# Optimization experiments

Hardware: AMD Instinct MI355X
Metric: run time of the kernel (lower is better)

The kernel has to match this reference:

```python
import jax, jax.numpy as jnp
import numpy as np

B, S, D, H = 4, 2048, 1024, 16
PD = D // H  # projection (head) dim


def setup_inputs() -> dict:
    key = jax.random.key(0)
    ks = jax.random.split(key, 11)
    s = 1.0 / np.sqrt(D)
    return {
        "q": jax.random.normal(ks[0], (B, S, D), jnp.float32),
        "k": jax.random.normal(ks[1], (B, S, D), jnp.float32),
        "v": jax.random.normal(ks[2], (B, S, D), jnp.float32),
        "Wq": jax.random.normal(ks[3], (D, D), jnp.float32) * s,
        "bq": jnp.zeros((D,), jnp.float32),
        "Wk": jax.random.normal(ks[4], (D, D), jnp.float32) * s,
        "bk": jnp.zeros((D,), jnp.float32),
        "Wv": jax.random.normal(ks[5], (D, D), jnp.float32) * s,
        "bv": jnp.zeros((D,), jnp.float32),
        "Wo": jax.random.normal(ks[6], (D, D), jnp.float32) * s,
        "bo": jnp.zeros((D,), jnp.float32),
        "use_causal_mask": 1,
    }


def _split_heads(x):
    # [B,S,D] -> [B,H,S,PD]
    return x.reshape(B, S, H, PD).transpose(0, 2, 1, 3)


def reference(q, k, v, Wq, bq, Wk, bk, Wv, bv, Wo, bo, use_causal_mask):
    qh = _split_heads(q @ Wq + bq)
    kh = _split_heads(k @ Wk + bk)
    vh = _split_heads(v @ Wv + bv)
    # scaled dot-product attention, O(S^2) scores materialized as in original
    logits = jnp.einsum("bhsd,bhtd->bhst", qh, kh) / jnp.sqrt(jnp.float32(PD))
    if use_causal_mask:
        # Faithful to original (buggy) mask: band_part lower-tri ones, then
        # logits += log(mask*1e-6 + 1.0) -- adds ~1e-6 where allowed, 0 where masked.
        mask = jnp.tril(jnp.ones((S, S), jnp.float32))
        logits = logits + jnp.log(mask * 1e-6 + 1.0)
    attn = jax.nn.softmax(logits, axis=-1)
    out = jnp.einsum("bhst,bhtd->bhsd", attn, vh)
    concat = out.transpose(0, 2, 1, 3).reshape(B, S, D)
    return concat @ Wo + bo
```

## Files before the change

kernel.cpp:

```cpp
#include <hip/hip_runtime.h>

#define B_ 4
#define S_ 2048
#define D_ 1024
#define H_ 16
#define PD_ 64
#define M_ 8192
#define QSCALE 0.180336880145787f

typedef __attribute__((ext_vector_type(8))) short s16x8;
typedef __attribute__((ext_vector_type(4))) short s16x4;
typedef __attribute__((ext_vector_type(4))) float f32x4;

__device__ __forceinline__ short f2bf(float f) {
    unsigned int u = __float_as_uint(f);
    u = (u + 0x7FFFu + ((u >> 16) & 1u)) >> 16;
    return (short)u;
}

__device__ __forceinline__ unsigned int cvt_pk_bf16(float lo, float hi) {
    unsigned int r;
    asm("v_cvt_pk_bf16_f32 %0, %1, %2" : "=v"(r) : "v"(lo), "v"(hi));
    return r;
}

#if __has_builtin(__builtin_amdgcn_exp2f)
__device__ __forceinline__ float fast_exp2(float x) { return __builtin_amdgcn_exp2f(x); }
#else
__device__ __forceinline__ float fast_exp2(float x) {
    float r;
    asm("v_exp_f32 %0, %1" : "=v"(r) : "v"(x));
    return r;
}
#endif

#define MFMA(a, b, c) __builtin_amdgcn_mfma_f32_16x16x32_bf16(a, b, c, 0, 0, 0)

__device__ __forceinline__ void gload16(const short* g, short* l) {
    __builtin_amdgcn_global_load_lds(
        (const __attribute__((address_space(1))) void*)g,
        (__attribute__((address_space(3))) void*)l, 16, 0, 0);
}

__global__ __launch_bounds__(256) void prep_kernel(
    const float* __restrict__ q, const float* __restrict__ k, const float* __restrict__ v,
    const float* __restrict__ Wq, const float* __restrict__ Wk,
    const float* __restrict__ Wv, const float* __restrict__ Wo,
    short* __restrict__ oq, short* __restrict__ ok, short* __restrict__ ov,
    short* __restrict__ wt) {
    __shared__ float tile[32][33];
    const int id = blockIdx.x;
    const int tid = threadIdx.x;
    if (id < 3072) {
        const int z = id >> 10, x = id & 1023;
        const float* X = (z == 0) ? q : (z == 1) ? k : v;
        short* out = (z == 0) ? oq : (z == 1) ? ok : ov;
        const float s = (z == 0) ? QSCALE : 1.0f;
        size_t i0 = ((size_t)x * 256 + tid) * 8;
        const size_t stride = (size_t)1024 * 256 * 8;
#pragma unroll
        for (int it = 0; it < 4; it++, i0 += stride) {
            float4 f0 = *(const float4*)&X[i0];
            float4 f1 = *(const float4*)&X[i0 + 4];
            s16x8 o = {f2bf(f0.x * s), f2bf(f0.y * s), f2bf(f0.z * s), f2bf(f0.w * s),
                       f2bf(f1.x * s), f2bf(f1.y * s), f2bf(f1.z * s), f2bf(f1.w * s)};
            *(s16x8*)&out[i0] = o;
        }
    } else {
        int t = id - 3072;
        const int z = t >> 10;
        t &= 1023;
        const float* W = (z == 0) ? Wq : (z == 1) ? Wk : (z == 2) ? Wv : Wo;
        short* out = wt + (size_t)z * (D_ * D_);
        const int k0 = (t >> 5) * 32, n0 = (t & 31) * 32;
        const int tx = tid & 31, ty = tid >> 5;
#pragma unroll
        for (int i = 0; i < 4; i++)
            tile[ty + 8 * i][tx] = W[(size_t)(k0 + ty + 8 * i) * D_ + n0 + tx];
        __syncthreads();
#pragma unroll
        for (int i = 0; i < 4; i++)
            out[(size_t)(n0 + ty + 8 * i) * D_ + k0 + tx] = f2bf(tile[tx][ty + 8 * i]);
    }
}

__device__ __forceinline__ void gemm_core(const short* __restrict__ A,
                                          const short* __restrict__ Bm,
                                          int bm, int bn, short* lds,
                                          f32x4 acc[4][4]) {
    const int tid = threadIdx.x;
    const int lane = tid & 63, wid = tid >> 6;
    const int wr = (wid >> 1) * 64, wc = (wid & 1) * 64;
    const int l15 = lane & 15, l4 = lane >> 4;

    const int rr = tid >> 2;
    const int cc = tid & 3;
    const int csw = (cc ^ ((rr >> 1) & 3)) * 8;
    const short* ap = A + (size_t)(bm + rr) * D_ + csw;
    const short* bp = Bm + (size_t)(bn + rr) * D_ + csw;
    const int ldw = wid * 512;

    const int ard = (l4 ^ ((l15 >> 1) & 3)) * 8;

#define PSTAGE(bi, kkc)                                                  \
    do {                                                                 \
        short* Lp = lds + (bi) * 8192;                                   \
        gload16(ap + (kkc), Lp + ldw);                                   \
        gload16(ap + (size_t)64 * D_ + (kkc), Lp + 2048 + ldw);          \
        gload16(bp + (kkc), Lp + 4096 + ldw);                            \
        gload16(bp + (size_t)64 * D_ + (kkc), Lp + 6144 + ldw);          \
    } while (0)

    PSTAGE(0, 0);
    PSTAGE(1, 32);

    int cur = 0;
    for (int t = 0; t < 32; t++) {
        if (t + 2 < 32) {
            int nb = cur + 2;
            if (nb >= 3) nb -= 3;
            PSTAGE(nb, (t + 2) * 32);
        }
        if (t <= 29)
            asm volatile("s_waitcnt vmcnt(8)" ::: "memory");
        else if (t == 30)
            asm volatile("s_waitcnt vmcnt(4)" ::: "memory");
        else
            asm volatile("s_waitcnt vmcnt(0)" ::: "memory");
        __builtin_amdgcn_s_barrier();

        const short* La = lds + cur * 8192;
        const short* Lb = La + 4096;
        s16x8 af[4], bf[4];
#pragma unroll
        for (int i = 0; i < 4; i++)
            af[i] = *(const s16x8*)&La[(wr + i * 16 + l15) * 32 + ard];
#pragma unroll
        for (int j = 0; j < 4; j++)
            bf[j] = *(const s16x8*)&Lb[(wc + j * 16 + l15) * 32 + ard];
#pragma unroll
        for (int i = 0; i < 4; i++)
#pragma unroll
            for (int j = 0; j < 4; j++)
                acc[i][j] = MFMA(bf[j], af[i], acc[i][j]);

        __builtin_amdgcn_s_barrier();
        cur = (cur == 2) ? 0 : cur + 1;
    }
#undef PSTAGE
}

__global__ __launch_bounds__(256) void proj_kernel(
    const short* __restrict__ xq, const short* __restrict__ xk, const short* __restrict__ xv,
    const float* __restrict__ bq, const float* __restrict__ bk, const float* __restrict__ bv,
    const short* __restrict__ wtbase, short* __restrict__ outQ, short* __restrict__ outK,
    short* __restrict__ outVT) {
    const int id = blockIdx.x;
    const int xcd = id & 7, slot = id >> 3;
    const int sb = xcd + 8 * (slot >> 6);
    const int wi = slot & 63;
    const int z = sb >> 3;
    const int bn = (wi & 7) * 128;
    const int bm = (((sb & 7) << 3) + (wi >> 3)) * 128;

    const short* A = (z == 0) ? xq : (z == 1) ? xk : xv;
    const float* bias = (z == 0) ? bq : (z == 1) ? bk : bv;
    const short* Wt = wtbase + (size_t)z * (D_ * D_);
    const float bscale = (z == 0) ? QSCALE : 1.0f;

    __shared__ __align__(16) short lds[3 * 8192];

    const int tid = threadIdx.x;
    const int lane = tid & 63, wid = tid >> 6;
    const int wr = (wid >> 1) * 64, wc = (wid & 1) * 64;
    const int l15 = lane & 15, l4 = lane >> 4;

    f32x4 acc[4][4];
#pragma unroll
    for (int i = 0; i < 4; i++)
#pragma unroll
        for (int j = 0; j < 4; j++) acc[i][j] = (f32x4){0.f, 0.f, 0.f, 0.f};

    gemm_core(A, Wt, bm, bn, lds, acc);

    if (z == 2) {
        const int b = bm >> 11, sbase = bm & (S_ - 1);
        short* T = lds;
        for (int chunk = 0; chunk < 4; chunk++) {
            __syncthreads();
            if ((wc >> 6) == (chunk >> 1)) {
                const int jbase = (chunk & 1) * 2;
#pragma unroll
                for (int jj = 0; jj < 2; jj++) {
                    const int j = jbase + jj;
                    float4 b4 = *(const float4*)&bias[bn + wc + j * 16 + l4 * 4];
                    const int prow = jj * 16 + l4 * 4;
#pragma unroll
                    for (int i = 0; i < 4; i++) {
                        const int sc2 = wr + i * 16 + l15;
                        T[(prow + 0) * 132 + sc2] = f2bf(acc[i][j][0] + b4.x);
                        T[(prow + 1) * 132 + sc2] = f2bf(acc[i][j][1] + b4.y);
                        T[(prow + 2) * 132 + sc2] = f2bf(acc[i][j][2] + b4.z);
                        T[(prow + 3) * 132 + sc2] = f2bf(acc[i][j][3] + b4.w);
                    }
                }
            }
            __syncthreads();
#pragma unroll
            for (int pass = 0; pass < 2; pass++) {
                const int r = pass * 16 + (tid >> 4);
                const int sc3 = (tid & 15) * 8;
                s16x8 vv = *(const s16x8*)&T[r * 132 + sc3];
                const int grow = b * 1024 + bn + chunk * 32 + r;
                const int kvg = sc3 & 64;
                const int c8 = (sc3 >> 3) & 7;
                const int hh2 = (c8 >> 2) * 32;
                const int m4 = ((c8 >> 1) & 1) * 4;
                const int posA = hh2 + 8 * ((2 * c8) & 3) + m4;
                const int posB = hh2 + 8 * ((2 * c8 + 1) & 3) + m4;
                const int sx = (r & 7) << 3;
                const s16x4* hv = (const s16x4*)&vv;
                const size_t base = (size_t)grow * S_ + sbase + kvg;
                *(s16x4*)&outVT[base + (posA ^ sx)] = hv[0];
                *(s16x4*)&outVT[base + (posB ^ sx)] = hv[1];
            }
        }
    } else {
        short* out = (z == 0) ? outQ : outK;
#pragma unroll
        for (int i = 0; i < 4; i++) {
            const int m = bm + wr + i * 16 + l15;
            const int b = m >> 11, s = m & (S_ - 1);
#pragma unroll
            for (int j = 0; j < 4; j++) {
                const int n = bn + wc + j * 16 + l4 * 4;
                float4 b4 = *(const float4*)&bias[n];
                s16x4 st;
                st[0] = f2bf(acc[i][j][0] + b4.x * bscale);
                st[1] = f2bf(acc[i][j][1] + b4.y * bscale);
                st[2] = f2bf(acc[i][j][2] + b4.z * bscale);
                st[3] = f2bf(acc[i][j][3] + b4.w * bscale);
                const int h = n >> 6, pd = n & 63;
                const int pdsw = (z == 1) ? (pd ^ ((s & 7) << 3)) : pd;
                *(s16x4*)&out[(((size_t)(b * H_ + h)) * S_ + s) * PD_ + pdsw] = st;
            }
        }
    }
}

__global__ __launch_bounds__(512, 4) void attn_kernel(
    const short* __restrict__ Qh, const short* __restrict__ Kh,
    const short* __restrict__ Vtg, short* __restrict__ aout) {
    const int did = blockIdx.x + gridDim.x * blockIdx.y;
    const int bh = (did & 7) * 8 + ((did >> 3) & 7);
    const int q0 = (did >> 6) * 128;
    const short* Qp = Qh + (size_t)bh * (S_ * PD_);
    const short* Kp = Kh + (size_t)bh * (S_ * PD_);
    const short* Vp = Vtg + (size_t)bh * (PD_ * S_);

    const int tid = threadIdx.x;
    const int lane = tid & 63, w = tid >> 6;
    const int l15 = lane & 15, l4 = lane >> 4;
    const int swz = (l15 & 7) << 3;

    __shared__ __align__(16) short Ks[3][64 * 64];
    __shared__ __align__(16) short Vs[3][64 * 64];

    s16x8 qf[2];
#pragma unroll
    for (int kk = 0; kk < 2; kk++)
        qf[kk] = *(const s16x8*)&Qp[(size_t)(q0 + w * 16 + l15) * PD_ + kk * 32 + l4 * 8];

    const s16x8 ones8 = {(short)0x3F80, (short)0x3F80, (short)0x3F80, (short)0x3F80,
                         (short)0x3F80, (short)0x3F80, (short)0x3F80, (short)0x3F80};

    f32x4 oacc[4];
#pragma unroll
    for (int i = 0; i < 4; i++) oacc[i] = (f32x4){0.f, 0.f, 0.f, 0.f};
    f32x4 sacc = (f32x4){0.f, 0.f, 0.f, 0.f};

    const short* kbase = Kp + (size_t)(tid >> 3) * PD_ + (tid & 7) * 8;
    const short* vbase = Vp + (size_t)(tid >> 3) * S_ + (tid & 7) * 8;
    const int ldw = w * 512;

#define AISSUE(bsel, st)                                              \
    do {                                                              \
        gload16(kbase + (size_t)(st) * (64 * PD_), &Ks[bsel][ldw]);   \
        gload16(vbase + (st) * 64, &Vs[bsel][ldw]);                   \
    } while (0)

    AISSUE(0, 0);
    AISSUE(1, 1);

    int cur = 0;
    for (int t = 0; t < 32; t++) {
        if (t < 31)
            asm volatile("s_waitcnt vmcnt(2)" ::: "memory");
        else
            asm volatile("s_waitcnt vmcnt(0)" ::: "memory");
        __syncthreads();
        if (t + 2 < 32) {
            int nb = cur + 2;
            if (nb >= 3) nb -= 3;
            AISSUE(nb, t + 2);
        }
        const short* Kc = Ks[cur];
        const short* Vc = Vs[cur];

        f32x4 s4[4];
#pragma unroll
        for (int n4 = 0; n4 < 4; n4++) s4[n4] = (f32x4){0.f, 0.f, 0.f, 0.f};
        __builtin_amdgcn_s_setprio(1);
#pragma unroll
        for (int n4 = 0; n4 < 4; n4++)
#pragma unroll
            for (int kk = 0; kk < 2; kk++) {
                s16x8 kf = *(const s16x8*)&Kc[(n4 * 16 + l15) * 64 + ((kk * 32 + l4 * 8) ^ swz)];
                s4[n4] = MFMA(kf, qf[kk], s4[n4]);
            }
        __builtin_amdgcn_s_setprio(0);

        s16x8 pb[2];
#pragma unroll
        for (int h = 0; h < 2; h++) {
            float p0 = fast_exp2(s4[2 * h][0]);
            float p1 = fast_exp2(s4[2 * h][1]);
            float p2 = fast_exp2(s4[2 * h][2]);
            float p3 = fast_exp2(s4[2 * h][3]);
            float p4 = fast_exp2(s4[2 * h + 1][0]);
            float p5 = fast_exp2(s4[2 * h + 1][1]);
            float p6 = fast_exp2(s4[2 * h + 1][2]);
            float p7 = fast_exp2(s4[2 * h + 1][3]);
            union { uint4 u; s16x8 s; } pu;
            pu.u.x = cvt_pk_bf16(p0, p1);
            pu.u.y = cvt_pk_bf16(p2, p3);
            pu.u.z = cvt_pk_bf16(p4, p5);
            pu.u.w = cvt_pk_bf16(p6, p7);
            pb[h] = pu.s;
            sacc = MFMA(ones8, pb[h], sacc);
        }

        __builtin_amdgcn_s_setprio(1);
#pragma unroll
        for (int i = 0; i < 4; i++) {
            const int vrow = (i * 16 + l15) * 64;
            s16x8 v0 = *(const s16x8*)&Vc[vrow + ((8 * l4) ^ swz)];
            s16x8 v1 = *(const s16x8*)&Vc[vrow + ((32 + 8 * l4) ^ swz)];
            oacc[i] = MFMA(v0, pb[0], oacc[i]);
            oacc[i] = MFMA(v1, pb[1], oacc[i]);
        }
        __builtin_amdgcn_s_setprio(0);
        cur = (cur == 2) ? 0 : cur + 1;
    }
#undef AISSUE

    const float inv = 1.0f / sacc[0];
    const int qrow = q0 + w * 16 + l15;
    const int bb = bh >> 4, hh = bh & 15;
#pragma unroll
    for (int i = 0; i < 4; i++) {
        s16x4 st;
        st[0] = f2bf(oacc[i][0] * inv);
        st[1] = f2bf(oacc[i][1] * inv);
        st[2] = f2bf(oacc[i][2] * inv);
        st[3] = f2bf(oacc[i][3] * inv);
        *(s16x4*)&aout[((size_t)(bb * S_ + qrow)) * D_ + hh * PD_ + i * 16 + l4 * 4] = st;
    }
}

__global__ __launch_bounds__(256) void out_kernel(
    const short* __restrict__ A, const short* __restrict__ Wt,
    const float* __restrict__ bo, float* __restrict__ out) {
    __shared__ __align__(16) short lds[3 * 8192];

    const int bm = blockIdx.x * 128, bn = blockIdx.y * 128;
    const int tid = threadIdx.x;
    const int lane = tid & 63, wid = tid >> 6;
    const int wr = (wid >> 1) * 64, wc = (wid & 1) * 64;
    const int l15 = lane & 15, l4 = lane >> 4;

    f32x4 acc[4][4];
#pragma unroll
    for (int i = 0; i < 4; i++)
#pragma unroll
        for (int j = 0; j < 4; j++) acc[i][j] = (f32x4){0.f, 0.f, 0.f, 0.f};

    gemm_core(A, Wt, bm, bn, lds, acc);

#pragma unroll
    for (int i = 0; i < 4; i++) {
        const int m = bm + wr + i * 16 + l15;
#pragma unroll
        for (int j = 0; j < 4; j++) {
            const int n = bn + wc + j * 16 + l4 * 4;
            float4 b4 = *(const float4*)&bo[n];
            float4 st;
            st.x = acc[i][j][0] + b4.x;
            st.y = acc[i][j][1] + b4.y;
            st.z = acc[i][j][2] + b4.z;
            st.w = acc[i][j][3] + b4.w;
            *(float4*)&out[(size_t)m * D_ + n] = st;
        }
    }
}

extern "C" void kernel_launch(void* const* d_in, const int* in_sizes, int n_in,
                              void* d_out, int out_size, void* d_ws, size_t ws_size,
                              hipStream_t stream) {
    const float* q  = (const float*)d_in[0];
    const float* k  = (const float*)d_in[1];
    const float* v  = (const float*)d_in[2];
    const float* Wq = (const float*)d_in[3];
    const float* bq = (const float*)d_in[4];
    const float* Wk = (const float*)d_in[5];
    const float* bk = (const float*)d_in[6];
    const float* Wv = (const float*)d_in[7];
    const float* bv = (const float*)d_in[8];
    const float* Wo = (const float*)d_in[9];
    const float* bo = (const float*)d_in[10];

    const size_t TEN = (size_t)M_ * D_;
    short* ws  = (short*)d_ws;
    short* wt  = ws;
    short* qh  = ws + 4 * (size_t)D_ * D_;
    short* kh  = qh + TEN;
    short* vtg = kh + TEN;
    short* xbk = vtg + TEN;
    short* xbv = xbk + TEN;
    short* xbq = (short*)d_out;
    short* ao  = xbk;
    float* out = (float*)d_out;

    hipLaunchKernelGGL(prep_kernel, dim3(7168, 1, 1), dim3(256, 1, 1), 0, stream,
                       q, k, v, Wq, Wk, Wv, Wo, xbq, xbk, xbv, wt);
    hipLaunchKernelGGL(proj_kernel, dim3(1536, 1, 1), dim3(256, 1, 1), 0, stream,
                       xbq, xbk, xbv, bq, bk, bv, wt, qh, kh, vtg);
    hipLaunchKernelGGL(attn_kernel, dim3(16, 64, 1), dim3(512, 1, 1), 0, stream,
                       qh, kh, vtg, ao);
    hipLaunchKernelGGL(out_kernel, dim3(64, 8, 1), dim3(256, 1, 1), 0, stream,
                       ao, wt + (size_t)3 * D_ * D_, bo, out);
}
```

Before: 229.4 us.

## Fuse fp32-to-bf16 activation conversion into projection GEMM A-tile loading

Removes the separate pass that converted q/k/v activations from fp32 to bf16 (and applied the Q scale) into workspace. The projection GEMM now reads fp32 activations directly into registers, scales and packs them to bf16, and writes them into swizzled LDS, with a new double-buffered pipeline replacing the three-stage async copy for A. This avoids writing and re-reading 3x8192x1024 bf16 tensors, at the cost of doubled A-operand global reads per GEMM tile (each A row is re-read by 8 column blocks in fp32) and a shallower, register-staged pipeline.

```diff
diff --git a/kernel.cpp b/kernel.cpp
--- a/kernel.cpp
+++ b/kernel.cpp
@@ -43,45 +43,25 @@
 }
 
 __global__ __launch_bounds__(256) void prep_kernel(
-    const float* __restrict__ q, const float* __restrict__ k, const float* __restrict__ v,
     const float* __restrict__ Wq, const float* __restrict__ Wk,
     const float* __restrict__ Wv, const float* __restrict__ Wo,
-    short* __restrict__ oq, short* __restrict__ ok, short* __restrict__ ov,
     short* __restrict__ wt) {
     __shared__ float tile[32][33];
     const int id = blockIdx.x;
     const int tid = threadIdx.x;
-    if (id < 3072) {
-        const int z = id >> 10, x = id & 1023;
-        const float* X = (z == 0) ? q : (z == 1) ? k : v;
-        short* out = (z == 0) ? oq : (z == 1) ? ok : ov;
-        const float s = (z == 0) ? QSCALE : 1.0f;
-        size_t i0 = ((size_t)x * 256 + tid) * 8;
-        const size_t stride = (size_t)1024 * 256 * 8;
-#pragma unroll
-        for (int it = 0; it < 4; it++, i0 += stride) {
-            float4 f0 = *(const float4*)&X[i0];
-            float4 f1 = *(const float4*)&X[i0 + 4];
-            s16x8 o = {f2bf(f0.x * s), f2bf(f0.y * s), f2bf(f0.z * s), f2bf(f0.w * s),
-                       f2bf(f1.x * s), f2bf(f1.y * s), f2bf(f1.z * s), f2bf(f1.w * s)};
-            *(s16x8*)&out[i0] = o;
-        }
-    } else {
-        int t = id - 3072;
-        const int z = t >> 10;
-        t &= 1023;
-        const float* W = (z == 0) ? Wq : (z == 1) ? Wk : (z == 2) ? Wv : Wo;
-        short* out = wt + (size_t)z * (D_ * D_);
-        const int k0 = (t >> 5) * 32, n0 = (t & 31) * 32;
-        const int tx = tid & 31, ty = tid >> 5;
-#pragma unroll
-        for (int i = 0; i < 4; i++)
-            tile[ty + 8 * i][tx] = W[(size_t)(k0 + ty + 8 * i) * D_ + n0 + tx];
-        __syncthreads();
-#pragma unroll
-        for (int i = 0; i < 4; i++)
-            out[(size_t)(n0 + ty + 8 * i) * D_ + k0 + tx] = f2bf(tile[tx][ty + 8 * i]);
-    }
+    const int z = id >> 10;
+    const int t = id & 1023;
+    const float* W = (z == 0) ? Wq : (z == 1) ? Wk : (z == 2) ? Wv : Wo;
+    short* out = wt + (size_t)z * (D_ * D_);
+    const int k0 = (t >> 5) * 32, n0 = (t & 31) * 32;
+    const int tx = tid & 31, ty = tid >> 5;
+#pragma unroll
+    for (int i = 0; i < 4; i++)
+        tile[ty + 8 * i][tx] = W[(size_t)(k0 + ty + 8 * i) * D_ + n0 + tx];
+    __syncthreads();
+#pragma unroll
+    for (int i = 0; i < 4; i++)
+        out[(size_t)(n0 + ty + 8 * i) * D_ + k0 + tx] = f2bf(tile[tx][ty + 8 * i]);
 }
 
 __device__ __forceinline__ void gemm_core(const short* __restrict__ A,
@@ -150,8 +130,113 @@
 #undef PSTAGE
 }
 
+__device__ __forceinline__ void gemm_core_f32(const float* __restrict__ Af,
+                                              float ascale,
+                                              const short* __restrict__ Bm,
+                                              int bm, int bn, short* lds,
+                                              f32x4 acc[4][4]) {
+    const int tid = threadIdx.x;
+    const int lane = tid & 63, wid = tid >> 6;
+    const int wr = (wid >> 1) * 64, wc = (wid & 1) * 64;
+    const int l15 = lane & 15, l4 = lane >> 4;
+
+    const int rr = tid >> 1, half = tid & 1;
+    const float* ap = Af + (size_t)(bm + rr) * D_ + half * 16;
+    const int aswz = (rr >> 1) & 3;
+    const int awoff0 = rr * 32 + (((half * 2) ^ aswz) * 8);
+    const int awoff1 = rr * 32 + (((half * 2 + 1) ^ aswz) * 8);
+
+    const int rrb = tid >> 2, ccb = tid & 3;
+    const int cswb = (ccb ^ ((rrb >> 1) & 3)) * 8;
+    const short* bp = Bm + (size_t)(bn + rrb) * D_ + cswb;
+    const int ldwb = wid * 512;
+
+    const int ard = (l4 ^ ((l15 >> 1) & 3)) * 8;
+
+    float4 ra0[4], ra1[4];
+
+#define ALOAD0(st)                                   \
+    do {                                             \
+        const float* p = ap + (st) * 32;             \
+        ra0[0] = *(const float4*)(p);                \
+        ra0[1] = *(const float4*)(p + 4);            \
+        ra0[2] = *(const float4*)(p + 8);            \
+        ra0[3] = *(const float4*)(p + 12);           \
+    } while (0)
+#define ALOAD1(st)                                   \
+    do {                                             \
+        const float* p = ap + (st) * 32;             \
+        ra1[0] = *(const float4*)(p);                \
+        ra1[1] = *(const float4*)(p + 4);            \
+        ra1[2] = *(const float4*)(p + 8);            \
+        ra1[3] = *(const float4*)(p + 12);           \
+    } while (0)
+#define BLOAD(buf, st)                                                      \
+    do {                                                                    \
+        short* Bp = lds + 8192 + (buf) * 4096;                              \
+        gload16(bp + (st) * 32, Bp + ldwb);                                 \
+        gload16(bp + (size_t)64 * D_ + (st) * 32, Bp + 2048 + ldwb);        \
+    } while (0)
+
+#define GBODY(T, CUR, RA, ALOADN)                                              \
+    do {                                                                       \
+        if ((T) < 31)                                                          \
+            asm volatile("s_waitcnt vmcnt(4)" ::: "memory");                   \
+        else                                                                   \
+            asm volatile("s_waitcnt vmcnt(0)" ::: "memory");                   \
+        short* Ac = lds + (CUR) * 4096;                                        \
+        {                                                                      \
+            union { uint4 u; s16x8 s; } c0, c1;                                \
+            c0.u.x = cvt_pk_bf16(RA[0].x * ascale, RA[0].y * ascale);          \
+            c0.u.y = cvt_pk_bf16(RA[0].z * ascale, RA[0].w * ascale);          \
+            c0.u.z = cvt_pk_bf16(RA[1].x * ascale, RA[1].y * ascale);          \
+            c0.u.w = cvt_pk_bf16(RA[1].z * ascale, RA[1].w * ascale);          \
+            c1.u.x = cvt_pk_bf16(RA[2].x * ascale, RA[2].y * ascale);          \
+            c1.u.y = cvt_pk_bf16(RA[2].z * ascale, RA[2].w * ascale);          \
+            c1.u.z = cvt_pk_bf16(RA[3].x * ascale, RA[3].y * ascale);          \
+            c1.u.w = cvt_pk_bf16(RA[3].z * ascale, RA[3].w * ascale);          \
+            *(s16x8*)&Ac[awoff0] = c0.s;                                       \
+            *(s16x8*)&Ac[awoff1] = c1.s;                                       \
+        }                                                                      \
+        asm volatile("s_waitcnt lgkmcnt(0)" ::: "memory");                     \
+        __builtin_amdgcn_s_barrier();                                          \
+        if ((T) + 1 < 32) BLOAD(1 - (CUR), (T) + 1);                           \
+        if ((T) + 2 < 32) ALOADN((T) + 2);                                     \
+        {                                                                      \
+            const short* La = lds + (CUR) * 4096;                              \
+            const short* Lb = lds + 8192 + (CUR) * 4096;                       \
+            s16x8 af[4], bf[4];                                                \
+            _Pragma("unroll")                                                  \
+            for (int i = 0; i < 4; i++)                                        \
+                af[i] = *(const s16x8*)&La[(wr + i * 16 + l15) * 32 + ard];    \
+            _Pragma("unroll")                                                  \
+            for (int j = 0; j < 4; j++)                                        \
+                bf[j] = *(const s16x8*)&Lb[(wc + j * 16 + l15) * 32 + ard];    \
+            _Pragma("unroll")                                                  \
+            for (int i = 0; i < 4; i++)                                        \
+                _Pragma("unroll")                                              \
+                for (int j = 0; j < 4; j++)                                    \
+                    acc[i][j] = MFMA(bf[j], af[i], acc[i][j]);                 \
+        }                                                                      \
+        __builtin_amdgcn_s_barrier();                                          \
+    } while (0)
+
+    ALOAD0(0);
+    BLOAD(0, 0);
+    ALOAD1(1);
+
+    for (int tt = 0; tt < 32; tt += 2) {
+        GBODY(tt, 0, ra0, ALOAD0);
+        GBODY(tt + 1, 1, ra1, ALOAD1);
+    }
+#undef GBODY
+#undef ALOAD0
+#undef ALOAD1
+#undef BLOAD
+}
+
 __global__ __launch_bounds__(256) void proj_kernel(
-    const short* __restrict__ xq, const short* __restrict__ xk, const short* __restrict__ xv,
+    const float* __restrict__ qf, const float* __restrict__ kf, const float* __restrict__ vf,
     const float* __restrict__ bq, const float* __restrict__ bk, const float* __restrict__ bv,
     const short* __restrict__ wtbase, short* __restrict__ outQ, short* __restrict__ outK,
     short* __restrict__ outVT) {
@@ -163,12 +248,13 @@
     const int bn = (wi & 7) * 128;
     const int bm = (((sb & 7) << 3) + (wi >> 3)) * 128;
 
-    const short* A = (z == 0) ? xq : (z == 1) ? xk : xv;
+    const float* A = (z == 0) ? qf : (z == 1) ? kf : vf;
     const float* bias = (z == 0) ? bq : (z == 1) ? bk : bv;
     const short* Wt = wtbase + (size_t)z * (D_ * D_);
+    const float ascale = (z == 0) ? QSCALE : 1.0f;
     const float bscale = (z == 0) ? QSCALE : 1.0f;
 
-    __shared__ __align__(16) short lds[3 * 8192];
+    __shared__ __align__(16) short lds[16384];
 
     const int tid = threadIdx.x;
     const int lane = tid & 63, wid = tid >> 6;
@@ -181,7 +267,7 @@
 #pragma unroll
         for (int j = 0; j < 4; j++) acc[i][j] = (f32x4){0.f, 0.f, 0.f, 0.f};
 
-    gemm_core(A, Wt, bm, bn, lds, acc);
+    gemm_core_f32(A, ascale, Wt, bm, bn, lds, acc);
 
     if (z == 2) {
         const int b = bm >> 11, sbase = bm & (S_ - 1);
@@ -425,16 +511,13 @@
     short* qh  = ws + 4 * (size_t)D_ * D_;
     short* kh  = qh + TEN;
     short* vtg = kh + TEN;
-    short* xbk = vtg + TEN;
-    short* xbv = xbk + TEN;
-    short* xbq = (short*)d_out;
-    short* ao  = xbk;
+    short* ao  = vtg + TEN;
     float* out = (float*)d_out;
 
-    hipLaunchKernelGGL(prep_kernel, dim3(7168, 1, 1), dim3(256, 1, 1), 0, stream,
-                       q, k, v, Wq, Wk, Wv, Wo, xbq, xbk, xbv, wt);
+    hipLaunchKernelGGL(prep_kernel, dim3(4096, 1, 1), dim3(256, 1, 1), 0, stream,
+                       Wq, Wk, Wv, Wo, wt);
     hipLaunchKernelGGL(proj_kernel, dim3(1536, 1, 1), dim3(256, 1, 1), 0, stream,
-                       xbq, xbk, xbv, bq, bk, bv, wt, qh, kh, vtg);
+                       q, k, v, bq, bk, bv, wt, qh, kh, vtg);
     hipLaunchKernelGGL(attn_kernel, dim3(16, 64, 1), dim3(512, 1, 1), 0, stream,
                        qh, kh, vtg, ao);
     hipLaunchKernelGGL(out_kernel, dim3(64, 8, 1), dim3(256, 1, 1), 0, stream,
```

Result: slower. 277.5 us (+21.0%).
